# Kernel tuning notes

Measured on AMD Instinct MI355X. Metric: run time of the kernel, lower is better.

## Reference

```python
import jax, jax.numpy as jnp
import numpy as np

T, B, I, H, O = 64, 1024, 64, 256, 1


def setup_inputs() -> dict:
    key = jax.random.key(0)
    ks = jax.random.split(key, 8)
    k = 1.0 / np.sqrt(H)  # torch RNN/Linear default init bound
    u = lambda kk, sh: jax.random.uniform(kk, sh, jnp.float32, -k, k)
    return {
        'data': jax.random.normal(ks[0], (T, B, I), jnp.float32),
        'nine_target_index': jax.random.randint(ks[1], (B, 9), 0, B + 1),  # B == outside-target pad row
        'haven_flag': 0,
        'h0': jnp.zeros((B, H), jnp.float32),  # init_hidden (layer dim squeezed)
        'W_ih': u(ks[2], (H, I)),
        'W_hh': u(ks[3], (H, H)),
        'b_ih': u(ks[4], (H,)),
        'b_hh': u(ks[5], (H,)),
        'W_lin': u(ks[6], (O, 2 * H)),
        'b_lin': u(ks[7], (O,)),
    }


def _forward(data, nine_target_index, haven_flag, h0, W_ih, W_hh, b_ih, b_hh, W_lin, b_lin):
    # --- vanilla relu RNN over time (seq-first layout, 1 layer) ---
    def step(h, x):
        h = jax.nn.relu(x @ W_ih.T + b_ih + h @ W_hh.T + b_hh)
        return h, h
    _, hs = jax.lax.scan(step, h0, data)          # (T, B, H) == hidden_output

    # Original code detaches hidden states before the numpy attention round-trip:
    hd = jax.lax.stop_gradient(hs)
    # pad batch dim with one zero 'outside target' row, then gather 3x3 neighborhoods
    h_pad = jnp.concatenate([hd, jnp.zeros((hd.shape[0], 1, H), hd.dtype)], axis=1)  # (T, B+1, H)
    gathered = h_pad[:, nine_target_index]        # (T, B, 9, H)  past_ht per timestep
    if haven_flag == 1:
        gathered = jnp.concatenate(
            [gathered, jnp.zeros(gathered.shape[:2] + (1, H), gathered.dtype)], axis=2)

    # scores[i, j, b, n] = <past_ht[j, b, n, :], ht[i, b, :]>  (query also detached in original)
    scores = jnp.einsum('jbnh,ibh->ijbn', gathered, hd)
    attn = jax.nn.softmax(scores, axis=-1)        # softmax over the 9 neighbors (dim=2 in torch)
    Tn = hs.shape[0]
    # c[i] = sum over strictly-past timesteps j < i of the attention-weighted neighbor states
    mask = jnp.tril(jnp.ones((Tn, Tn), attn.dtype), -1)       # mask[i, j] = 1 iff j < i
    attn_m = attn * mask[:, :, None, None]
    c_rest = jnp.einsum('ijbn,jbnh->ibh', attn_m, gathered)   # (T, B, H)
    # i == 0 with LAG=='ALL': c[0] = hidden_output[0] (NOT detached in original)
    c = jnp.concatenate([hs[:1], c_rest[1:]], axis=0)

    concat = jnp.concatenate([c, hs], axis=-1)    # (T, B, 2H)
    pred = jax.nn.relu(concat @ W_lin.T + b_lin)  # (T, B, O)
    return pred, attn


def reference(data, nine_target_index, haven_flag, h0, W_ih, W_hh, b_ih, b_hh, W_lin, b_lin):
    return _forward(data, nine_target_index, haven_flag, h0, W_ih, W_hh, b_ih, b_hh, W_lin, b_lin)
```

## Files before the change

### kernel.cpp

```cpp
#include <hip/hip_runtime.h>

#define T_ 64
#define B_ 1024
#define I_ 64
#define H_ 256

typedef short bf16x8 __attribute__((ext_vector_type(8)));
typedef float f32x4 __attribute__((ext_vector_type(4)));

#define MFMA16(a, b, c) __builtin_amdgcn_mfma_f32_16x16x32_bf16((a), (b), (c), 0, 0, 0)

__device__ __forceinline__ float bf2f(unsigned short u) {
    union { unsigned int i; float f; } x;
    x.i = ((unsigned int)u) << 16;
    return x.f;
}
__device__ __forceinline__ unsigned short f2bf(float f) {
    union { float f; unsigned int i; } x;
    x.f = f;
    unsigned int u = x.i;
    unsigned int r = u + 0x7FFFu + ((u >> 16) & 1u);
    return (unsigned short)(r >> 16);
}
__device__ __forceinline__ void split8(const float* p, bf16x8& hi, bf16x8& lo) {
#pragma unroll
    for (int q = 0; q < 8; ++q) {
        float f = p[q];
        unsigned short h1 = f2bf(f);
        hi[q] = (short)h1;
        lo[q] = (short)f2bf(f - bf2f(h1));
    }
}

__global__ __launch_bounds__(512) void rnn_kernel(
    const float* __restrict__ data,
    const float* __restrict__ h0,
    const float* __restrict__ Wih, const float* __restrict__ Whh,
    const float* __restrict__ bih, const float* __restrict__ bhh,
    unsigned short* __restrict__ hsHi, unsigned short* __restrict__ hsLo)
{
    __shared__ unsigned short hbuf[2][2][16 * 264];
    __shared__ float bsum[H_];

    const int tid  = threadIdx.x;
    const int lane = tid & 63;
    const int w    = tid >> 6;
    const int quad = lane >> 4;
    const int l15  = lane & 15;
    const int b0   = blockIdx.x * 16;

    bf16x8 whhH[2][8], whhL[2][8], wihH[2][2], wihL[2][2];
#pragma unroll
    for (int it = 0; it < 2; ++it) {
        int n = (w * 2 + it) * 16 + l15;
#pragma unroll
        for (int kc = 0; kc < 8; ++kc)
            split8(Whh + (size_t)n * H_ + kc * 32 + quad * 8, whhH[it][kc], whhL[it][kc]);
#pragma unroll
        for (int kx = 0; kx < 2; ++kx)
            split8(Wih + (size_t)n * I_ + kx * 32 + quad * 8, wihH[it][kx], wihL[it][kx]);
    }

    if (tid < H_) bsum[tid] = bih[tid] + bhh[tid];
    {
        int r  = tid >> 5;
        int hh = (tid & 31) * 8;
        const float* src = h0 + (size_t)(b0 + r) * H_ + hh;
#pragma unroll
        for (int q = 0; q < 8; ++q) {
            float f = src[q];
            unsigned short hi = f2bf(f);
            hbuf[0][0][r * 264 + hh + q] = hi;
            hbuf[0][1][r * 264 + hh + q] = f2bf(f - bf2f(hi));
        }
    }
    __syncthreads();

    float xf[16];
    {
        const float* dp = data + ((size_t)(b0 + l15)) * I_ + quad * 8;
#pragma unroll
        for (int q = 0; q < 8; ++q) { xf[q] = dp[q]; xf[8 + q] = dp[32 + q]; }
    }

    int cur = 0;
    for (int t = 0; t < T_; ++t) {
        bf16x8 xhi[2], xlo[2];
#pragma unroll
        for (int kx = 0; kx < 2; ++kx)
#pragma unroll
            for (int q = 0; q < 8; ++q) {
                float f = xf[kx * 8 + q];
                unsigned short h1 = f2bf(f);
                xhi[kx][q] = (short)h1;
                xlo[kx][q] = (short)f2bf(f - bf2f(h1));
            }
        if (t + 1 < T_) {
            const float* dp = data + ((size_t)(t + 1) * B_ + b0 + l15) * I_ + quad * 8;
#pragma unroll
            for (int q = 0; q < 8; ++q) { xf[q] = dp[q]; xf[8 + q] = dp[32 + q]; }
        }

        f32x4 cA[2], cB[2], cC[2];
#pragma unroll
        for (int it = 0; it < 2; ++it) {
            cA[it] = (f32x4){0.f, 0.f, 0.f, 0.f};
            cB[it] = (f32x4){0.f, 0.f, 0.f, 0.f};
            cC[it] = (f32x4){0.f, 0.f, 0.f, 0.f};
        }

#pragma unroll
        for (int kx = 0; kx < 2; ++kx) {
#pragma unroll
            for (int it = 0; it < 2; ++it) cA[it] = MFMA16(xhi[kx], wihH[it][kx], cA[it]);
#pragma unroll
            for (int it = 0; it < 2; ++it) cB[it] = MFMA16(xhi[kx], wihL[it][kx], cB[it]);
#pragma unroll
            for (int it = 0; it < 2; ++it) cC[it] = MFMA16(xlo[kx], wihH[it][kx], cC[it]);
        }
#pragma unroll
        for (int kc = 0; kc < 8; ++kc) {
            bf16x8 ahi = *(const bf16x8*)&hbuf[cur][0][l15 * 264 + kc * 32 + quad * 8];
            bf16x8 alo = *(const bf16x8*)&hbuf[cur][1][l15 * 264 + kc * 32 + quad * 8];
#pragma unroll
            for (int it = 0; it < 2; ++it) cA[it] = MFMA16(ahi, whhH[it][kc], cA[it]);
#pragma unroll
            for (int it = 0; it < 2; ++it) cB[it] = MFMA16(ahi, whhL[it][kc], cB[it]);
#pragma unroll
            for (int it = 0; it < 2; ++it) cC[it] = MFMA16(alo, whhH[it][kc], cC[it]);
        }

        int nxt = cur ^ 1;
#pragma unroll
        for (int it = 0; it < 2; ++it) {
            int h = (w * 2 + it) * 16 + l15;
            float bs = bsum[h];
#pragma unroll
            for (int reg = 0; reg < 4; ++reg) {
                int r = quad * 4 + reg;
                float v = (cA[it][reg] + cB[it][reg] + cC[it][reg]) + bs;
                v = fmaxf(v, 0.f);
                unsigned short hi = f2bf(v);
                unsigned short lo = f2bf(v - bf2f(hi));
                hbuf[nxt][0][r * 264 + h] = hi;
                hbuf[nxt][1][r * 264 + h] = lo;
            }
        }
        __syncthreads();
        {
            int r  = tid >> 5;
            int hc = (tid & 31) * 8;
            size_t g = ((size_t)t * B_ + b0 + r) * H_ + hc;
            *(bf16x8*)(hsHi + g) = *(const bf16x8*)&hbuf[nxt][0][r * 264 + hc];
            *(bf16x8*)(hsLo + g) = *(const bf16x8*)&hbuf[nxt][1][r * 264 + hc];
        }
        cur = nxt;
    }
}

__global__ __launch_bounds__(256) void attn_kernel(
    const unsigned short* __restrict__ hsHi,
    const unsigned short* __restrict__ hsLo,
    const int* __restrict__ nti,
    const float* __restrict__ Wlin,
    const float* __restrict__ blin,
    float* __restrict__ outPred,
    float* __restrict__ outAttn)
{
    __shared__ unsigned short GpH[18 * 264];
    __shared__ unsigned short GpL[18 * 264];
    __shared__ unsigned short GpT[256 * 40];
    __shared__ float predc[64];
    __shared__ int   sidx[9];
    __shared__ float blin_s;

    const int tid  = threadIdx.x;
    const int lane = tid & 63;
    const int w    = tid >> 6;
    const int quad = lane >> 4;
    const int l15  = lane & 15;
    const int b    = blockIdx.x;

    if (tid == 0) blin_s = blin[0];
    if (tid < 9) sidx[tid] = nti[b * 9 + tid];
    for (int e = tid; e < 256 * 14; e += 256) {
        int h = e / 14, c = 18 + e % 14;
        GpT[h * 40 + c] = 0;
    }

    bf16x8 af[8], afl[8];
    {
        size_t base = ((size_t)(w * 16 + l15) * B_ + b) * H_;
#pragma unroll
        for (int kc = 0; kc < 8; ++kc) {
            af[kc]  = *(const bf16x8*)(hsHi + base + kc * 32 + quad * 8);
            afl[kc] = *(const bf16x8*)(hsLo + base + kc * 32 + quad * 8);
        }
    }
    f32x4 acc[16];
#pragma unroll
    for (int nt = 0; nt < 16; ++nt) acc[nt] = (f32x4){0.f, 0.f, 0.f, 0.f};
    __syncthreads();

    ushort4 gh0[3], gl0[3], gh1[3], gl1[3];

#define ISSUE_GATHER(P)                                                        \
    {                                                                          \
        int j0g = 2 * (P);                                                     \
        _Pragma("unroll")                                                      \
        for (int c = 0; c < 3; ++c) {                                          \
            int n = w + 4 * c;                                                 \
            if (n < 9) {                                                       \
                int bi = sidx[n];                                              \
                if (bi < B_) {                                                 \
                    size_t base0 = ((size_t)j0g * B_ + bi) * H_;               \
                    size_t base1 = base0 + (size_t)B_ * H_;                    \
                    gh0[c] = ((const ushort4*)(hsHi + base0))[lane];           \
                    gl0[c] = ((const ushort4*)(hsLo + base0))[lane];           \
                    gh1[c] = ((const ushort4*)(hsHi + base1))[lane];           \
                    gl1[c] = ((const ushort4*)(hsLo + base1))[lane];           \
                } else {                                                       \
                    gh0[c].x=gh0[c].y=gh0[c].z=gh0[c].w=0;                     \
                    gl0[c].x=gl0[c].y=gl0[c].z=gl0[c].w=0;                     \
                    gh1[c].x=gh1[c].y=gh1[c].z=gh1[c].w=0;                     \
                    gl1[c].x=gl1[c].y=gl1[c].z=gl1[c].w=0;                     \
                }                                                              \
            }                                                                  \
        }                                                                      \
    }

    ISSUE_GATHER(0);

    for (int p = 0; p < 32; ++p) {
        int j0 = 2 * p;
        if (p) __syncthreads();
#pragma unroll
        for (int c = 0; c < 3; ++c) {
            int n = w + 4 * c;
            if (n < 9) {
                *(ushort4*)&GpH[n * 264 + lane * 4]       = gh0[c];
                *(ushort4*)&GpL[n * 264 + lane * 4]       = gl0[c];
                *(ushort4*)&GpH[(9 + n) * 264 + lane * 4] = gh1[c];
                *(ushort4*)&GpL[(9 + n) * 264 + lane * 4] = gl1[c];
                unsigned short h0v[4] = {gh0[c].x, gh0[c].y, gh0[c].z, gh0[c].w};
                unsigned short h1v[4] = {gh1[c].x, gh1[c].y, gh1[c].z, gh1[c].w};
#pragma unroll
                for (int q = 0; q < 4; ++q) {
                    ushort2 pr2; pr2.x = h0v[q]; pr2.y = h1v[q];
                    *(ushort2*)&GpT[(lane + q * 64) * 40 + 2 * n] = pr2;
                }
            }
        }
        if (p < 31) ISSUE_GATHER(p + 1);
        __syncthreads();

        unsigned short pmreg[2][4];
#pragma unroll
        for (int jslot = 0; jslot < 2; ++jslot) {
            int j = j0 + jslot;
            int ar = jslot * 9 + l15;
            ar = (ar < 18) ? ar : 17;
            f32x4 sA = (f32x4){0.f, 0.f, 0.f, 0.f};
            f32x4 sB = (f32x4){0.f, 0.f, 0.f, 0.f};
            f32x4 sC = (f32x4){0.f, 0.f, 0.f, 0.f};
#pragma unroll
            for (int kc = 0; kc < 8; ++kc) {
                bf16x8 aH = *(const bf16x8*)&GpH[ar * 264 + kc * 32 + quad * 8];
                bf16x8 aL = *(const bf16x8*)&GpL[ar * 264 + kc * 32 + quad * 8];
                sA = MFMA16(aH, af[kc],  sA);
                sB = MFMA16(aH, afl[kc], sB);
                sC = MFMA16(aL, af[kc],  sC);
            }
            f32x4 s = sA + sB + sC;
            int i = w * 16 + l15;
            int nvalid = (quad < 2) ? 4 : ((quad == 2) ? 1 : 0);
            float mp = -1e30f;
#pragma unroll
            for (int r = 0; r < 4; ++r) if (r < nvalid) mp = fmaxf(mp, s[r]);
            mp = fmaxf(mp, __shfl_xor(mp, 16, 64));
            mp = fmaxf(mp, __shfl_xor(mp, 32, 64));
            float e[4], sp = 0.f;
#pragma unroll
            for (int r = 0; r < 4; ++r) {
                e[r] = (r < nvalid) ? __expf(s[r] - mp) : 0.f;
                sp += e[r];
            }
            sp += __shfl_xor(sp, 16, 64);
            sp += __shfl_xor(sp, 32, 64);
            float inv = 1.f / sp;
#pragma unroll
            for (int r = 0; r < 4; ++r) {
                pmreg[jslot][r] = 0;
                if (r < nvalid) {
                    int n = quad * 4 + r;
                    float pr = e[r] * inv;
                    outAttn[(((size_t)i * T_ + j) * B_ + b) * 9 + n] = pr;
                    pmreg[jslot][r] = (j < i) ? f2bf(pr) : (unsigned short)0;
                }
            }
        }

        {
            bf16x8 afp;
#pragma unroll
            for (int q = 0; q < 8; ++q) afp[q] = (short)pmreg[q & 1][q >> 1];
            const int prow_base = (l15 >> 2) + (l15 & 3) * 64;
#pragma unroll
            for (int nt = 0; nt < 16; ++nt) {
                bf16x8 bfg = *(const bf16x8*)&GpT[(prow_base + nt * 4) * 40 + quad * 8];
                acc[nt] = MFMA16(afp, bfg, acc[nt]);
            }
        }
    }

    float hw1 = 0.f, hw2 = 0.f;
#pragma unroll
    for (int kc = 0; kc < 8; ++kc) {
#pragma unroll
        for (int jj = 0; jj < 8; ++jj) {
            float hv = bf2f((unsigned short)af[kc][jj]) + bf2f((unsigned short)afl[kc][jj]);
            int h = kc * 32 + quad * 8 + jj;
            hw1 += hv * Wlin[h];
            hw2 += hv * Wlin[H_ + h];
        }
    }
    hw1 += __shfl_xor(hw1, 16, 64); hw1 += __shfl_xor(hw1, 32, 64);
    hw2 += __shfl_xor(hw2, 16, 64); hw2 += __shfl_xor(hw2, 32, 64);

#pragma unroll
    for (int reg = 0; reg < 4; ++reg) {
        float cp = 0.f;
#pragma unroll
        for (int nt = 0; nt < 16; ++nt)
            cp += acc[nt][reg] * Wlin[nt * 16 + l15];
        for (int m = 8; m >= 1; m >>= 1) cp += __shfl_xor(cp, m, 16);
        if (l15 == 0) predc[w * 16 + quad * 4 + reg] = cp;
    }
    __syncthreads();
    if (lane < 16) {
        int i = w * 16 + lane;
        float v = predc[i] + hw2 + ((i == 0) ? hw1 : 0.f) + blin_s;
        v = fmaxf(v, 0.f);
        outPred[(size_t)i * B_ + b] = v;
    }
}

extern "C" void kernel_launch(void* const* d_in, const int* in_sizes, int n_in,
                              void* d_out, int out_size, void* d_ws, size_t ws_size,
                              hipStream_t stream) {
    (void)in_sizes; (void)n_in; (void)out_size; (void)ws_size;
    const float* data = (const float*)d_in[0];
    const int*   nti  = (const int*)d_in[1];
    const float* h0   = (const float*)d_in[3];
    const float* Wih  = (const float*)d_in[4];
    const float* Whh  = (const float*)d_in[5];
    const float* bih  = (const float*)d_in[6];
    const float* bhh  = (const float*)d_in[7];
    const float* Wlin = (const float*)d_in[8];
    const float* blin = (const float*)d_in[9];

    unsigned short* ws = (unsigned short*)d_ws;
    unsigned short* hsHi = ws;
    unsigned short* hsLo = ws + (size_t)T_ * B_ * H_;

    float* outPred = (float*)d_out;
    float* outAttn = (float*)d_out + (size_t)T_ * B_;

    rnn_kernel<<<dim3(64), dim3(512), 0, stream>>>(data, h0, Wih, Whh, bih, bhh, hsHi, hsLo);
    attn_kernel<<<dim3(1024), dim3(256), 0, stream>>>(hsHi, hsLo, nti, Wlin, blin,
                                                      outPred, outAttn);
}
```

Baseline: 555.4 us.

## Split RNN recurrence across 16 waves with one output tile each

The RNN block grows from 8 to 16 waves, so each wave computes one 16-wide hidden tile instead of two. This shortens the per-step serial MFMA chain and halves register use for the resident weights. The input load is now issued inside the step, and its MFMAs run after the recurrent ones so the load latency can hide behind them; the previous cross-step prefetch is dropped. The cost is more waves contending for the per-step barrier and narrower global stores.

```diff
diff --git a/kernel.cpp b/kernel.cpp
--- a/kernel.cpp
+++ b/kernel.cpp
@@ -32,7 +32,7 @@
     }
 }
 
-__global__ __launch_bounds__(512) void rnn_kernel(
+__global__ __launch_bounds__(1024) void rnn_kernel(
     const float* __restrict__ data,
     const float* __restrict__ h0,
     const float* __restrict__ Wih, const float* __restrict__ Whh,
@@ -49,25 +49,24 @@
     const int l15  = lane & 15;
     const int b0   = blockIdx.x * 16;
 
-    bf16x8 whhH[2][8], whhL[2][8], wihH[2][2], wihL[2][2];
-#pragma unroll
-    for (int it = 0; it < 2; ++it) {
-        int n = (w * 2 + it) * 16 + l15;
+    bf16x8 whhH[8], whhL[8], wihH[2], wihL[2];
+    {
+        int n = w * 16 + l15;
 #pragma unroll
         for (int kc = 0; kc < 8; ++kc)
-            split8(Whh + (size_t)n * H_ + kc * 32 + quad * 8, whhH[it][kc], whhL[it][kc]);
+            split8(Whh + (size_t)n * H_ + kc * 32 + quad * 8, whhH[kc], whhL[kc]);
 #pragma unroll
         for (int kx = 0; kx < 2; ++kx)
-            split8(Wih + (size_t)n * I_ + kx * 32 + quad * 8, wihH[it][kx], wihL[it][kx]);
+            split8(Wih + (size_t)n * I_ + kx * 32 + quad * 8, wihH[kx], wihL[kx]);
     }
 
     if (tid < H_) bsum[tid] = bih[tid] + bhh[tid];
     {
-        int r  = tid >> 5;
-        int hh = (tid & 31) * 8;
+        int r  = tid >> 6;
+        int hh = (tid & 63) * 4;
         const float* src = h0 + (size_t)(b0 + r) * H_ + hh;
 #pragma unroll
-        for (int q = 0; q < 8; ++q) {
+        for (int q = 0; q < 4; ++q) {
             float f = src[q];
             unsigned short hi = f2bf(f);
             hbuf[0][0][r * 264 + hh + q] = hi;
@@ -76,69 +75,54 @@
     }
     __syncthreads();
 
-    float xf[16];
-    {
-        const float* dp = data + ((size_t)(b0 + l15)) * I_ + quad * 8;
-#pragma unroll
-        for (int q = 0; q < 8; ++q) { xf[q] = dp[q]; xf[8 + q] = dp[32 + q]; }
-    }
-
     int cur = 0;
     for (int t = 0; t < T_; ++t) {
-        bf16x8 xhi[2], xlo[2];
-#pragma unroll
-        for (int kx = 0; kx < 2; ++kx)
-#pragma unroll
-            for (int q = 0; q < 8; ++q) {
-                float f = xf[kx * 8 + q];
-                unsigned short h1 = f2bf(f);
-                xhi[kx][q] = (short)h1;
-                xlo[kx][q] = (short)f2bf(f - bf2f(h1));
-            }
-        if (t + 1 < T_) {
-            const float* dp = data + ((size_t)(t + 1) * B_ + b0 + l15) * I_ + quad * 8;
+        float xf[16];
+        {
+            const float* dp = data + ((size_t)t * B_ + b0 + l15) * I_ + quad * 8;
 #pragma unroll
             for (int q = 0; q < 8; ++q) { xf[q] = dp[q]; xf[8 + q] = dp[32 + q]; }
         }
 
-        f32x4 cA[2], cB[2], cC[2];
-#pragma unroll
-        for (int it = 0; it < 2; ++it) {
-            cA[it] = (f32x4){0.f, 0.f, 0.f, 0.f};
-            cB[it] = (f32x4){0.f, 0.f, 0.f, 0.f};
-            cC[it] = (f32x4){0.f, 0.f, 0.f, 0.f};
-        }
-
-#pragma unroll
-        for (int kx = 0; kx < 2; ++kx) {
-#pragma unroll
-            for (int it = 0; it < 2; ++it) cA[it] = MFMA16(xhi[kx], wihH[it][kx], cA[it]);
-#pragma unroll
-            for (int it = 0; it < 2; ++it) cB[it] = MFMA16(xhi[kx], wihL[it][kx], cB[it]);
-#pragma unroll
-            for (int it = 0; it < 2; ++it) cC[it] = MFMA16(xlo[kx], wihH[it][kx], cC[it]);
-        }
+        f32x4 cA = (f32x4){0.f, 0.f, 0.f, 0.f};
+        f32x4 cB = (f32x4){0.f, 0.f, 0.f, 0.f};
+        f32x4 cC = (f32x4){0.f, 0.f, 0.f, 0.f};
+
 #pragma unroll
         for (int kc = 0; kc < 8; ++kc) {
             bf16x8 ahi = *(const bf16x8*)&hbuf[cur][0][l15 * 264 + kc * 32 + quad * 8];
             bf16x8 alo = *(const bf16x8*)&hbuf[cur][1][l15 * 264 + kc * 32 + quad * 8];
-#pragma unroll
-            for (int it = 0; it < 2; ++it) cA[it] = MFMA16(ahi, whhH[it][kc], cA[it]);
-#pragma unroll
-            for (int it = 0; it < 2; ++it) cB[it] = MFMA16(ahi, whhL[it][kc], cB[it]);
-#pragma unroll
-            for (int it = 0; it < 2; ++it) cC[it] = MFMA16(alo, whhH[it][kc], cC[it]);
+            cA = MFMA16(ahi, whhH[kc], cA);
+            cB = MFMA16(ahi, whhL[kc], cB);
+            cC = MFMA16(alo, whhH[kc], cC);
+        }
+        {
+            bf16x8 xhi[2], xlo[2];
+#pragma unroll
+            for (int kx = 0; kx < 2; ++kx)
+#pragma unroll
+                for (int q = 0; q < 8; ++q) {
+                    float f = xf[kx * 8 + q];
+                    unsigned short h1 = f2bf(f);
+                    xhi[kx][q] = (short)h1;
+                    xlo[kx][q] = (short)f2bf(f - bf2f(h1));
+                }
+#pragma unroll
+            for (int kx = 0; kx < 2; ++kx) {
+                cA = MFMA16(xhi[kx], wihH[kx], cA);
+                cB = MFMA16(xhi[kx], wihL[kx], cB);
+                cC = MFMA16(xlo[kx], wihH[kx], cC);
+            }
         }
 
         int nxt = cur ^ 1;
-#pragma unroll
-        for (int it = 0; it < 2; ++it) {
-            int h = (w * 2 + it) * 16 + l15;
+        {
+            int h = w * 16 + l15;
             float bs = bsum[h];
 #pragma unroll
             for (int reg = 0; reg < 4; ++reg) {
                 int r = quad * 4 + reg;
-                float v = (cA[it][reg] + cB[it][reg] + cC[it][reg]) + bs;
+                float v = (cA[reg] + cB[reg] + cC[reg]) + bs;
                 v = fmaxf(v, 0.f);
                 unsigned short hi = f2bf(v);
                 unsigned short lo = f2bf(v - bf2f(hi));
@@ -148,11 +132,11 @@
         }
         __syncthreads();
         {
-            int r  = tid >> 5;
-            int hc = (tid & 31) * 8;
+            int r  = tid >> 6;
+            int hc = (tid & 63) * 4;
             size_t g = ((size_t)t * B_ + b0 + r) * H_ + hc;
-            *(bf16x8*)(hsHi + g) = *(const bf16x8*)&hbuf[nxt][0][r * 264 + hc];
-            *(bf16x8*)(hsLo + g) = *(const bf16x8*)&hbuf[nxt][1][r * 264 + hc];
+            *(ushort4*)(hsHi + g) = *(const ushort4*)&hbuf[nxt][0][r * 264 + hc];
+            *(ushort4*)(hsLo + g) = *(const ushort4*)&hbuf[nxt][1][r * 264 + hc];
         }
         cur = nxt;
     }
@@ -366,7 +350,7 @@
     float* outPred = (float*)d_out;
     float* outAttn = (float*)d_out + (size_t)T_ * B_;
 
-    rnn_kernel<<<dim3(64), dim3(512), 0, stream>>>(data, h0, Wih, Whh, bih, bhh, hsHi, hsLo);
+    rnn_kernel<<<dim3(64), dim3(1024), 0, stream>>>(data, h0, Wih, Whh, bih, bhh, hsHi, hsLo);
     attn_kernel<<<dim3(1024), dim3(256), 0, stream>>>(hsHi, hsLo, nti, Wlin, blin,
                                                       outPred, outAttn);
 }
```

Measured after the change: 721.4 us. 29.9% more time.
